# Performance work log

Measured on AMD Instinct MI355X. Metric: run time of the kernel, lower is better.

Reference implementation:

```python
import jax, jax.numpy as jnp
import numpy as np

IN_SLICE = (4, 4)   # input bit-plane widths, MSB first
W_SLICE = (4, 4)    # weight bit-plane widths, MSB first
KSIZE, STRIDE, PAD = 3, 1, 1
B, CIN, COUT, H, W = 16, 64, 128, 32, 32


def _slice_planes(x, bits):
    """Dynamic fixed-point quantization to sum(bits) signed bits, then split
    the magnitude into bit-planes (sign folded into each plane). Exact:
    sum_i 2**shift_i * plane_i == q, and scale * q ~= x."""
    n = int(sum(bits))
    qmax = float(2 ** (n - 1) - 1)
    scale = jnp.max(jnp.abs(x)) / qmax
    q = jnp.clip(jnp.round(x / scale), -qmax, qmax)
    sgn = jnp.sign(q)
    u = jnp.abs(q)
    planes, shifts = [], []
    s = n
    for b in bits:
        s -= b
        planes.append(sgn * (jnp.floor(u / (2.0 ** s)) % (2.0 ** b)))
        shifts.append(s)
    return planes, shifts, scale


def _unfold(x, k, stride, pad):
    """torch.nn.functional.unfold, (C, kh, kw) channel-major ordering.
    Returns [B, L, C*k*k], Ho, Wo."""
    b, c, h, w = x.shape
    xp = jnp.pad(x, ((0, 0), (0, 0), (pad, pad), (pad, pad)))
    ho = (h + 2 * pad - k) // stride + 1
    wo = (w + 2 * pad - k) // stride + 1
    cols = []
    for kh in range(k):
        for kw in range(k):
            cols.append(xp[:, :, kh:kh + (ho - 1) * stride + 1:stride,
                            kw:kw + (wo - 1) * stride + 1:stride])
    patches = jnp.stack(cols, axis=2)              # [B, C, k*k, Ho, Wo]
    patches = patches.reshape(b, c * k * k, ho * wo)
    return patches.transpose(0, 2, 1), ho, wo      # [B, L, K]


def _mem_conv(input, weight, bias):
    cout = weight.shape[0]
    wm = weight.reshape(cout, -1).T                # [K, Cout], matches weight.reshape(Cout,-1).t()
    xun, ho, wo = _unfold(input, KSIZE, STRIDE, PAD)
    xplanes, xshifts, xscale = _slice_planes(xun, IN_SLICE)
    wplanes, wshifts, wscale = _slice_planes(wm, W_SLICE)
    acc = jnp.zeros((input.shape[0], xun.shape[1], cout), dtype=input.dtype)
    for xp, sx in zip(xplanes, xshifts):
        for wp, sw in zip(wplanes, wshifts):
            # low-precision bit-plane GEMM with power-of-two shift recombination
            acc = acc + (2.0 ** (sx + sw)) * jnp.einsum('blk,ko->blo', xp, wp)
    out = (xscale * wscale) * acc                  # [B, L, Cout]
    out = out.transpose(0, 2, 1).reshape(input.shape[0], cout, ho, wo)
    return out + bias[None, :, None, None]


def setup_inputs() -> dict:
    key = jax.random.key(0)
    k1, k2, k3 = jax.random.split(key, 3)
    x = jax.random.normal(k1, (B, CIN, H, W), dtype=jnp.float32)
    fan_in = CIN * KSIZE * KSIZE
    bound = 1.0 / np.sqrt(fan_in)  # kaiming_uniform(a=sqrt(5)) -> U(-1/sqrt(fan_in), +)
    weight = jax.random.uniform(k2, (COUT, CIN, KSIZE, KSIZE), dtype=jnp.float32,
                                minval=-bound, maxval=bound)
    bias = jax.random.uniform(k3, (COUT,), dtype=jnp.float32, minval=-bound, maxval=bound)
    return {"input": x, "weight": weight, "bias": bias}


def reference(input, weight, bias):
    return _mem_conv(input, weight, bias)
```

## Files before the change

kernel.cpp:

```cpp
#include <hip/hip_runtime.h>

#define B_    16
#define CIN   64
#define COUT  128
#define H_    32
#define W_    32
#define HP    34
#define NPB   128

typedef __attribute__((ext_vector_type(8)))  short  short8;
typedef __attribute__((ext_vector_type(16))) float  float16v;

__device__ __forceinline__ unsigned short f2bf(float q) {
  return (unsigned short)(__builtin_bit_cast(unsigned int, q) >> 16);
}

__device__ __forceinline__ float wave_max128(const float* __restrict__ p) {
  const int lane = threadIdx.x & 63;
  float m = fmaxf(p[lane], p[lane + 64]);
#pragma unroll
  for (int off = 32; off > 0; off >>= 1)
    m = fmaxf(m, __shfl_down(m, off, 64));
  return __shfl(m, 0, 64);
}

__global__ __launch_bounds__(256) void maxabs_kernel(
    const float4* __restrict__ x4, const float4* __restrict__ w4,
    float* __restrict__ bmx, float* __restrict__ bmw) {
  const int nx4 = B_ * CIN * H_ * W_ / 4;
  const int nw4 = COUT * CIN * 9 / 4;
  const int tid = blockIdx.x * 256 + threadIdx.x;
  const int stride = NPB * 256;
  float mx = 0.0f, mw = 0.0f;
  for (int i = tid; i < nx4; i += stride) {
    float4 v = x4[i];
    mx = fmaxf(mx, fmaxf(fmaxf(fabsf(v.x), fabsf(v.y)),
                         fmaxf(fabsf(v.z), fabsf(v.w))));
  }
  for (int i = tid; i < nw4; i += stride) {
    float4 v = w4[i];
    mw = fmaxf(mw, fmaxf(fmaxf(fabsf(v.x), fabsf(v.y)),
                         fmaxf(fabsf(v.z), fabsf(v.w))));
  }
#pragma unroll
  for (int off = 32; off > 0; off >>= 1) {
    mx = fmaxf(mx, __shfl_down(mx, off, 64));
    mw = fmaxf(mw, __shfl_down(mw, off, 64));
  }
  __shared__ float smx[4], smw[4];
  const int wid = threadIdx.x >> 6;
  if ((threadIdx.x & 63) == 0) { smx[wid] = mx; smw[wid] = mw; }
  __syncthreads();
  if (threadIdx.x == 0) {
#pragma unroll
    for (int i = 1; i < 4; ++i) { mx = fmaxf(mx, smx[i]); mw = fmaxf(mw, smw[i]); }
    bmx[blockIdx.x] = mx;
    bmw[blockIdx.x] = mw;
  }
}

__global__ __launch_bounds__(256) void quant_pack_kernel(
    const float* __restrict__ x, const float* __restrict__ w,
    const float* __restrict__ bmx, const float* __restrict__ bmw,
    unsigned short* __restrict__ qx, unsigned short* __restrict__ qw) {
  __shared__ __align__(16) unsigned short lds[W_ * 72];
  const int t = threadIdx.x;
  const int bb = blockIdx.x;
  if (bb < 512) {
    const int b = bb >> 5, y = bb & 31;
    const float s = wave_max128(bmx) / 127.0f;
#pragma unroll
    for (int k = 0; k < 8; ++k) {
      const int u = t + k * 256;
      const int cin = u >> 5, xx = u & 31;
      float q = rintf(x[((b * CIN + cin) * H_ + y) * W_ + xx] / s);
      q = fminf(fmaxf(q, -127.0f), 127.0f);
      lds[xx * 72 + cin] = f2bf(q);
    }
    __syncthreads();
    const int xx = t >> 3, c0 = (t & 7) * 8;
    *(uint4*)(qx + ((size_t)(b * HP + y + 1) * HP + xx + 1) * 64 + c0) =
        *(const uint4*)(&lds[xx * 72 + c0]);
  } else if (bb < 800) {
    const int i = (bb - 512) * 256 + t;
    const float s = wave_max128(bmw) / 127.0f;
    float q = rintf(w[i] / s);
    q = fminf(fmaxf(q, -127.0f), 127.0f);
    const int kw = i % 3; int j = i / 3;
    const int kh = j % 3; j /= 3;
    const int c = j & 63; const int o = j >> 6;
    qw[(kh * 3 + kw) * (COUT * CIN) + o * CIN + c] = f2bf(q);
  } else {
    const int v = (bb - 800) * 256 + t;
    const int b = v / 1056;
    const int r = v - b * 1056;
    const size_t base = (size_t)b * (HP * HP * 64);
    size_t off;
    if (r < 272)       off = base + (size_t)r * 8;
    else if (r < 544)  off = base + (size_t)33 * (HP * 64) + (size_t)(r - 272) * 8;
    else if (r < 800) {
      const int i2 = r - 544;
      off = base + (size_t)(1 + (i2 >> 3)) * (HP * 64) + (size_t)(i2 & 7) * 8;
    } else {
      const int i2 = r - 800;
      off = base + (size_t)(1 + (i2 >> 3)) * (HP * 64) + 33 * 64 + (size_t)(i2 & 7) * 8;
    }
    uint4 z; z.x = z.y = z.z = z.w = 0;
    *(uint4*)(qx + off) = z;
  }
}

__global__ __launch_bounds__(256, 2) void conv_mfma_kernel(
    const unsigned short* __restrict__ qx,
    const unsigned short* __restrict__ qw,
    const float* __restrict__ bmx, const float* __restrict__ bmw,
    const float* __restrict__ bias, float* __restrict__ out) {
  const int lane = threadIdx.x & 63;
  const int wv   = threadIdx.x >> 6;
  const int col  = lane & 31;
  const int kb   = lane >> 5;
  const int y    = blockIdx.x;
  const int b    = blockIdx.y;
  const int co0  = wv * 32;

  float16v acc0 = (float16v)0.0f, acc1 = (float16v)0.0f;

  const unsigned short* __restrict__ xb =
      qx + ((size_t)(b * HP + y) * HP + col) * 64 + kb * 8;
  const unsigned short* __restrict__ wb =
      qw + (size_t)(co0 + col) * 64 + kb * 8;

#pragma unroll
  for (int kh = 0; kh < 3; ++kh) {
#pragma unroll
    for (int kw = 0; kw < 3; ++kw) {
      const int s = kh * 3 + kw;
#pragma unroll
      for (int k16 = 0; k16 < 4; ++k16) {
        short8 a = *(const short8*)(wb + s * (COUT * CIN) + k16 * 16);
        short8 bf = *(const short8*)(xb + (kh * HP + kw) * 64 + k16 * 16);
        if (((s * 4 + k16) & 1) == 0)
          acc0 = __builtin_amdgcn_mfma_f32_32x32x16_bf16(a, bf, acc0, 0, 0, 0);
        else
          acc1 = __builtin_amdgcn_mfma_f32_32x32x16_bf16(a, bf, acc1, 0, 0, 0);
      }
    }
  }

  const float mx = wave_max128(bmx);
  const float mw = wave_max128(bmw);
  const float sc = (mx / 127.0f) * (mw / 127.0f);
  const float16v acc = acc0 + acc1;
#pragma unroll
  for (int r = 0; r < 16; ++r) {
    const int row  = (r & 3) + 8 * (r >> 2) + 4 * kb;
    const int cout = co0 + row;
    out[((b * COUT + cout) << 10) + y * W_ + col] = sc * acc[r] + bias[cout];
  }
}

extern "C" void kernel_launch(void* const* d_in, const int* in_sizes, int n_in,
                              void* d_out, int out_size, void* d_ws, size_t ws_size,
                              hipStream_t stream) {
  const float* x    = (const float*)d_in[0];
  const float* w    = (const float*)d_in[1];
  const float* bias = (const float*)d_in[2];
  float* out = (float*)d_out;

  float* bmx = (float*)d_ws;
  float* bmw = bmx + 128;
  unsigned short* qx = (unsigned short*)((char*)d_ws + 1024);
  unsigned short* qw = qx + (size_t)B_ * HP * HP * CIN;

  maxabs_kernel<<<NPB, 256, 0, stream>>>((const float4*)x, (const float4*)w,
                                         bmx, bmw);
  quant_pack_kernel<<<866, 256, 0, stream>>>(x, w, bmx, bmw, qx, qw);
  conv_mfma_kernel<<<dim3(32, 16), 256, 0, stream>>>(qx, qw, bmx, bmw, bias, out);
}
```

Measured before the change: 83.14 us.

## Repack quantized activations and weights into MFMA-fragment-contiguous layouts

Activations are now stored per padded row with a (k16, kb, x) ordering, and weights are stored grouped by (tap, k16, kb, cout). Each lane's short8 load for an MFMA fragment becomes contiguous across lanes instead of strided by 64 channels, and halo zeroing is folded into the per-row pack. The max-abs pass doubles its block count and fully unrolls a fixed four loads per thread. The cost is more complex indexing in the pack kernel and scattered 2-byte weight writes.

```diff
diff --git a/kernel.cpp b/kernel.cpp
--- a/kernel.cpp
+++ b/kernel.cpp
@@ -6,7 +6,8 @@
 #define H_    32
 #define W_    32
 #define HP    34
-#define NPB   128
+#define XROW  2176
+#define NPB   256
 
 typedef __attribute__((ext_vector_type(8)))  short  short8;
 typedef __attribute__((ext_vector_type(16))) float  float16v;
@@ -15,9 +16,10 @@
   return (unsigned short)(__builtin_bit_cast(unsigned int, q) >> 16);
 }
 
-__device__ __forceinline__ float wave_max128(const float* __restrict__ p) {
+__device__ __forceinline__ float wave_max256(const float* __restrict__ p) {
   const int lane = threadIdx.x & 63;
-  float m = fmaxf(p[lane], p[lane + 64]);
+  float m = fmaxf(fmaxf(p[lane], p[lane + 64]),
+                  fmaxf(p[lane + 128], p[lane + 192]));
 #pragma unroll
   for (int off = 32; off > 0; off >>= 1)
     m = fmaxf(m, __shfl_down(m, off, 64));
@@ -32,13 +34,14 @@
   const int tid = blockIdx.x * 256 + threadIdx.x;
   const int stride = NPB * 256;
   float mx = 0.0f, mw = 0.0f;
-  for (int i = tid; i < nx4; i += stride) {
-    float4 v = x4[i];
+#pragma unroll
+  for (int k = 0; k < 4; ++k) {
+    float4 v = x4[tid + k * stride];
     mx = fmaxf(mx, fmaxf(fmaxf(fabsf(v.x), fabsf(v.y)),
                          fmaxf(fabsf(v.z), fabsf(v.w))));
   }
-  for (int i = tid; i < nw4; i += stride) {
-    float4 v = w4[i];
+  if (tid < nw4) {
+    float4 v = w4[tid];
     mw = fmaxf(mw, fmaxf(fmaxf(fabsf(v.x), fabsf(v.y)),
                          fmaxf(fabsf(v.z), fabsf(v.w))));
   }
@@ -68,7 +71,7 @@
   const int bb = blockIdx.x;
   if (bb < 512) {
     const int b = bb >> 5, y = bb & 31;
-    const float s = wave_max128(bmx) / 127.0f;
+    const float s = wave_max256(bmx) / 127.0f;
 #pragma unroll
     for (int k = 0; k < 8; ++k) {
       const int u = t + k * 256;
@@ -78,35 +81,35 @@
       lds[xx * 72 + cin] = f2bf(q);
     }
     __syncthreads();
-    const int xx = t >> 3, c0 = (t & 7) * 8;
-    *(uint4*)(qx + ((size_t)(b * HP + y + 1) * HP + xx + 1) * 64 + c0) =
-        *(const uint4*)(&lds[xx * 72 + c0]);
-  } else if (bb < 800) {
-    const int i = (bb - 512) * 256 + t;
-    const float s = wave_max128(bmw) / 127.0f;
+    const size_t row = (size_t)(b * HP + y + 1) * XROW;
+    for (int c = t; c < 272; c += 256) {
+      const int k16 = c / 68;
+      const int r   = c - k16 * 68;
+      const int kbh = r / 34;
+      const int xs  = r - kbh * 34;
+      uint4 v; v.x = v.y = v.z = v.w = 0;
+      if (xs >= 1 && xs <= 32)
+        v = *(const uint4*)(&lds[(xs - 1) * 72 + k16 * 16 + kbh * 8]);
+      *(uint4*)(qx + row + (size_t)c * 8) = v;
+    }
+  } else if (bb < 544) {
+    const int idx = bb - 512;
+    const int b = idx >> 1, yy = (idx & 1) ? 33 : 0;
+    const size_t row = (size_t)(b * HP + yy) * XROW;
+    uint4 z; z.x = z.y = z.z = z.w = 0;
+    for (int c = t; c < 272; c += 256)
+      *(uint4*)(qx + row + (size_t)c * 8) = z;
+  } else {
+    const int i = (bb - 544) * 256 + t;
+    const float s = wave_max256(bmw) / 127.0f;
     float q = rintf(w[i] / s);
     q = fminf(fmaxf(q, -127.0f), 127.0f);
     const int kw = i % 3; int j = i / 3;
     const int kh = j % 3; j /= 3;
     const int c = j & 63; const int o = j >> 6;
-    qw[(kh * 3 + kw) * (COUT * CIN) + o * CIN + c] = f2bf(q);
-  } else {
-    const int v = (bb - 800) * 256 + t;
-    const int b = v / 1056;
-    const int r = v - b * 1056;
-    const size_t base = (size_t)b * (HP * HP * 64);
-    size_t off;
-    if (r < 272)       off = base + (size_t)r * 8;
-    else if (r < 544)  off = base + (size_t)33 * (HP * 64) + (size_t)(r - 272) * 8;
-    else if (r < 800) {
-      const int i2 = r - 544;
-      off = base + (size_t)(1 + (i2 >> 3)) * (HP * 64) + (size_t)(i2 & 7) * 8;
-    } else {
-      const int i2 = r - 800;
-      off = base + (size_t)(1 + (i2 >> 3)) * (HP * 64) + 33 * 64 + (size_t)(i2 & 7) * 8;
-    }
-    uint4 z; z.x = z.y = z.z = z.w = 0;
-    *(uint4*)(qx + off) = z;
+    const int sidx = kh * 3 + kw;
+    const int k16 = c >> 4, kb2 = (c >> 3) & 1, e = c & 7;
+    qw[(size_t)((((sidx * 4 + k16) * 2 + kb2) * 128 + o)) * 8 + e] = f2bf(q);
   }
 }
 
@@ -125,20 +128,21 @@
 
   float16v acc0 = (float16v)0.0f, acc1 = (float16v)0.0f;
 
-  const unsigned short* __restrict__ xb =
-      qx + ((size_t)(b * HP + y) * HP + col) * 64 + kb * 8;
-  const unsigned short* __restrict__ wb =
-      qw + (size_t)(co0 + col) * 64 + kb * 8;
+  const unsigned short* __restrict__ xp =
+      qx + (size_t)b * HP * XROW + kb * 272 + col * 8;
+  const unsigned short* __restrict__ wp =
+      qw + kb * 1024 + (co0 + col) * 8;
 
 #pragma unroll
   for (int kh = 0; kh < 3; ++kh) {
+    const unsigned short* __restrict__ xr = xp + (size_t)(y + kh) * XROW;
 #pragma unroll
     for (int kw = 0; kw < 3; ++kw) {
       const int s = kh * 3 + kw;
 #pragma unroll
       for (int k16 = 0; k16 < 4; ++k16) {
-        short8 a = *(const short8*)(wb + s * (COUT * CIN) + k16 * 16);
-        short8 bf = *(const short8*)(xb + (kh * HP + kw) * 64 + k16 * 16);
+        short8 a  = *(const short8*)(wp + (s * 4 + k16) * 2048);
+        short8 bf = *(const short8*)(xr + k16 * 544 + kw * 8);
         if (((s * 4 + k16) & 1) == 0)
           acc0 = __builtin_amdgcn_mfma_f32_32x32x16_bf16(a, bf, acc0, 0, 0, 0);
         else
@@ -147,8 +151,8 @@
     }
   }
 
-  const float mx = wave_max128(bmx);
-  const float mw = wave_max128(bmw);
+  const float mx = wave_max256(bmx);
+  const float mw = wave_max256(bmw);
   const float sc = (mx / 127.0f) * (mw / 127.0f);
   const float16v acc = acc0 + acc1;
 #pragma unroll
@@ -168,12 +172,12 @@
   float* out = (float*)d_out;
 
   float* bmx = (float*)d_ws;
-  float* bmw = bmx + 128;
-  unsigned short* qx = (unsigned short*)((char*)d_ws + 1024);
-  unsigned short* qw = qx + (size_t)B_ * HP * HP * CIN;
+  float* bmw = bmx + 256;
+  unsigned short* qx = (unsigned short*)((char*)d_ws + 2048);
+  unsigned short* qw = qx + (size_t)B_ * HP * XROW;
 
   maxabs_kernel<<<NPB, 256, 0, stream>>>((const float4*)x, (const float4*)w,
                                          bmx, bmw);
-  quant_pack_kernel<<<866, 256, 0, stream>>>(x, w, bmx, bmw, qx, qw);
+  quant_pack_kernel<<<832, 256, 0, stream>>>(x, w, bmx, bmw, qx, qw);
   conv_mfma_kernel<<<dim3(32, 16), 256, 0, stream>>>(qx, qw, bmx, bmw, bias, out);
 }
```

Result: faster. 75.85 us (-8.8%).
